# Optimization experiments

Hardware: AMD Instinct MI355X
Metric: run time of the kernel (lower is better)

Reference implementation:

```python
import jax, jax.numpy as jnp
import numpy as np

B, S, F, E, R, O = 4, 2048, 2048, 16, 16, 2048
TEMPERATURE = 1.0


def setup_inputs() -> dict:
    key = jax.random.key(0)
    k1, k2, k3, k4 = jax.random.split(key, 4)
    x = jax.random.normal(k1, (B, S, F), dtype=jnp.float32)
    prototypes = jax.random.normal(k2, (E, F), dtype=jnp.float32)
    # prototypes are top right-singular vectors -> unit norm rows
    prototypes = prototypes / jnp.linalg.norm(prototypes, axis=1, keepdims=True)
    A_stack = jax.random.normal(k3, (E, R, F), dtype=jnp.float32) * 0.02
    B_stack = jax.random.normal(k4, (E, O, R), dtype=jnp.float32) * 0.02
    scaling = jnp.float32(2.0)
    return {"x": x, "prototypes": prototypes, "A_stack": A_stack,
            "B_stack": B_stack, "scaling": scaling, "top_k": 4}


def reference(x, prototypes, A_stack, B_stack, scaling, top_k):
    lead = x.shape[:-1]
    f_in = x.shape[-1]
    tok = x.reshape(-1, f_in)                       # (t, F)
    t = tok.shape[0]

    # Arrow routing: abs cosine-like similarity to per-expert prototypes
    sim = jnp.abs(tok @ prototypes.T)               # (t, E)
    top_v, idx = jax.lax.top_k(sim, top_k)          # (t, k)
    full_score = jnp.full(sim.shape, -jnp.inf, dtype=sim.dtype)
    full_score = full_score.at[jnp.arange(t)[:, None], idx].set(top_v)
    coeff = jax.nn.softmax(full_score / TEMPERATURE, axis=1)  # (t, E), zeros off top-k

    # Per-expert LoRA: z = tok @ A_e^T  (dense over all experts, as in source)
    z = jnp.einsum('tf,erf->ter', tok, A_stack)     # (t, E, r)
    # Combine coeff into the low-rank space before the B projection to avoid
    # materializing the (t, E, out) tensor; math identical to
    # einsum('te, teo -> to', coeff, einsum('ter,eor->teo', z, B_stack)).
    delta = jnp.einsum('te,ter,eor->to', coeff, z, B_stack)  # (t, O)

    delta = scaling * delta                          # dropout = identity (eval)
    return delta.reshape(lead + (delta.shape[-1],))
```

## Files before the change

kernel.cpp:

```cpp
#include <hip/hip_runtime.h>
#include <hip/hip_bf16.h>
#include <stdint.h>

#define T_TOKENS 8192
#define F_DIM    2048
#define E_EXP    16
#define R_RANK   16
#define O_DIM    2048
#define KDIM     (E_EXP * R_RANK)

typedef short v8s __attribute__((ext_vector_type(8)));
typedef float v4f __attribute__((ext_vector_type(4)));

#define AS1 __attribute__((address_space(1)))
#define AS3 __attribute__((address_space(3)))

__device__ __forceinline__ uint16_t f2bf(float f) {
  uint32_t u = __builtin_bit_cast(uint32_t, f);
  u += 0x7fffu + ((u >> 16) & 1u);
  return (uint16_t)(u >> 16);
}

__device__ __forceinline__ void g2lds16(const uint16_t* g, uint16_t* l) {
  __builtin_amdgcn_global_load_lds((AS1 void*)g, (AS3 void*)l, 16, 0, 0);
}

__global__ __launch_bounds__(256) void prep_weights(
    const float* __restrict__ A, const float* __restrict__ Bst,
    uint16_t* __restrict__ Ab, uint16_t* __restrict__ Bb) {
  int idx = blockIdx.x * 256 + threadIdx.x;
  if (idx < KDIM * F_DIM) {
    Ab[idx] = f2bf(A[idx]);
  }
  if (idx < O_DIM * KDIM) {
    int k = idx & (KDIM - 1);
    int o = idx >> 8;
    int e = k >> 4, r = k & 15;
    Bb[idx] = f2bf(Bst[((size_t)e * O_DIM + o) * R_RANK + r]);
  }
}

__global__ __launch_bounds__(256) void route_stream(
    const float* __restrict__ x, const float* __restrict__ P,
    uint16_t* __restrict__ xb, float4* __restrict__ partials4) {
  __shared__ float ps[16 * 260];
  const int tid = threadIdx.x;
  const int c   = blockIdx.x;
  const int by  = blockIdx.y;
  const int f0  = c * 256;

  {
    const int e = tid >> 4;
    #pragma unroll
    for (int j = 0; j < 4; ++j) {
      const int col = (tid & 15) * 4 + j * 64;
      *(float4*)&ps[e * 260 + col] =
          *(const float4*)&P[(size_t)e * F_DIM + f0 + col];
    }
  }
  __syncthreads();

  const int sub = tid & 15;
  const int tg  = tid >> 4;
  const int t0  = by * 64 + tg * 4;
  const float* xr = x + (size_t)t0 * F_DIM + f0;
  uint16_t*    xw = xb + (size_t)t0 * F_DIM + f0;

  float a0[16], a1[16], a2[16], a3[16];
  #pragma unroll
  for (int e = 0; e < 16; ++e) { a0[e] = 0.f; a1[e] = 0.f; a2[e] = 0.f; a3[e] = 0.f; }

  #pragma unroll
  for (int j = 0; j < 4; ++j) {
    const int off = sub * 4 + j * 64;
    float4 v0 = *(const float4*)&xr[off];
    float4 v1 = *(const float4*)&xr[F_DIM + off];
    float4 v2 = *(const float4*)&xr[2 * F_DIM + off];
    float4 v3 = *(const float4*)&xr[3 * F_DIM + off];
    uint2 p0, p1, p2, p3;
    p0.x = (uint32_t)f2bf(v0.x) | ((uint32_t)f2bf(v0.y) << 16);
    p0.y = (uint32_t)f2bf(v0.z) | ((uint32_t)f2bf(v0.w) << 16);
    p1.x = (uint32_t)f2bf(v1.x) | ((uint32_t)f2bf(v1.y) << 16);
    p1.y = (uint32_t)f2bf(v1.z) | ((uint32_t)f2bf(v1.w) << 16);
    p2.x = (uint32_t)f2bf(v2.x) | ((uint32_t)f2bf(v2.y) << 16);
    p2.y = (uint32_t)f2bf(v2.z) | ((uint32_t)f2bf(v2.w) << 16);
    p3.x = (uint32_t)f2bf(v3.x) | ((uint32_t)f2bf(v3.y) << 16);
    p3.y = (uint32_t)f2bf(v3.z) | ((uint32_t)f2bf(v3.w) << 16);
    *(uint2*)&xw[off]             = p0;
    *(uint2*)&xw[F_DIM + off]     = p1;
    *(uint2*)&xw[2 * F_DIM + off] = p2;
    *(uint2*)&xw[3 * F_DIM + off] = p3;
    #pragma unroll
    for (int e = 0; e < 16; ++e) {
      float4 pv = *(float4*)&ps[e * 260 + off];
      a0[e] += v0.x * pv.x; a0[e] += v0.y * pv.y; a0[e] += v0.z * pv.z; a0[e] += v0.w * pv.w;
      a1[e] += v1.x * pv.x; a1[e] += v1.y * pv.y; a1[e] += v1.z * pv.z; a1[e] += v1.w * pv.w;
      a2[e] += v2.x * pv.x; a2[e] += v2.y * pv.y; a2[e] += v2.z * pv.z; a2[e] += v2.w * pv.w;
      a3[e] += v3.x * pv.x; a3[e] += v3.y * pv.y; a3[e] += v3.z * pv.z; a3[e] += v3.w * pv.w;
    }
  }

  #pragma unroll
  for (int e = 0; e < 16; ++e) {
    #pragma unroll
    for (int m = 1; m < 16; m <<= 1) {
      a0[e] += __shfl_xor(a0[e], m, 64);
      a1[e] += __shfl_xor(a1[e], m, 64);
      a2[e] += __shfl_xor(a2[e], m, 64);
      a3[e] += __shfl_xor(a3[e], m, 64);
    }
  }

  const size_t cb = (size_t)c * 4;
  if (sub == 0) {
    #pragma unroll
    for (int e4 = 0; e4 < 4; ++e4)
      partials4[(cb + e4) * T_TOKENS + t0] =
          make_float4(a0[e4 * 4], a0[e4 * 4 + 1], a0[e4 * 4 + 2], a0[e4 * 4 + 3]);
  } else if (sub == 1) {
    #pragma unroll
    for (int e4 = 0; e4 < 4; ++e4)
      partials4[(cb + e4) * T_TOKENS + t0 + 1] =
          make_float4(a1[e4 * 4], a1[e4 * 4 + 1], a1[e4 * 4 + 2], a1[e4 * 4 + 3]);
  } else if (sub == 2) {
    #pragma unroll
    for (int e4 = 0; e4 < 4; ++e4)
      partials4[(cb + e4) * T_TOKENS + t0 + 2] =
          make_float4(a2[e4 * 4], a2[e4 * 4 + 1], a2[e4 * 4 + 2], a2[e4 * 4 + 3]);
  } else if (sub == 3) {
    #pragma unroll
    for (int e4 = 0; e4 < 4; ++e4)
      partials4[(cb + e4) * T_TOKENS + t0 + 3] =
          make_float4(a3[e4 * 4], a3[e4 * 4 + 1], a3[e4 * 4 + 2], a3[e4 * 4 + 3]);
  }
}

__global__ __launch_bounds__(256) void route_topk(
    const float4* __restrict__ partials4, const float* __restrict__ scaling,
    const int* __restrict__ topk, float* __restrict__ coeffS) {
  const int t = blockIdx.x * 256 + threadIdx.x;
  double s[16];
  #pragma unroll
  for (int e = 0; e < 16; ++e) s[e] = 0.0;
  for (int c = 0; c < 8; ++c) {
    #pragma unroll
    for (int e4 = 0; e4 < 4; ++e4) {
      float4 p = partials4[((size_t)c * 4 + e4) * T_TOKENS + t];
      s[e4 * 4]     += (double)p.x;
      s[e4 * 4 + 1] += (double)p.y;
      s[e4 * 4 + 2] += (double)p.z;
      s[e4 * 4 + 3] += (double)p.w;
    }
  }
  double v[16];
  #pragma unroll
  for (int e = 0; e < 16; ++e) v[e] = fabs(s[e]);

  int k = topk[0];
  if (k > 16) k = 16;
  if (k < 1)  k = 1;
  unsigned mask = 0;
  double mx = 0.0;
  float ssum = 0.f;
  for (int i = 0; i < k; ++i) {
    double bv = -1.0; int bj = 0;
    #pragma unroll
    for (int j = 0; j < 16; ++j) {
      bool ok = !((mask >> j) & 1u) && (v[j] > bv);
      bv = ok ? v[j] : bv;
      bj = ok ? j  : bj;
    }
    mask |= 1u << bj;
    if (i == 0) mx = bv;
    ssum += expf((float)(bv - mx));
  }
  const float sc = scaling[0];
  float co[16];
  #pragma unroll
  for (int j = 0; j < 16; ++j)
    co[j] = ((mask >> j) & 1u) ? expf((float)(v[j] - mx)) / ssum * sc : 0.f;
  float* cw = coeffS + (size_t)t * 16;
  #pragma unroll
  for (int j4 = 0; j4 < 4; ++j4)
    *(float4*)&cw[j4 * 4] = make_float4(co[j4 * 4], co[j4 * 4 + 1],
                                        co[j4 * 4 + 2], co[j4 * 4 + 3]);
}

__global__ __launch_bounds__(256) void gemm_xa(
    const uint16_t* __restrict__ xb, const uint16_t* __restrict__ Ab,
    const float* __restrict__ coeffS, uint16_t* __restrict__ wb) {
  __shared__ uint16_t S[16384];
  uint16_t* Xh[2] = { S,         S + 4096  };
  uint16_t* Ah[2] = { S + 8192,  S + 12288 };
  const int tid  = threadIdx.x;
  const int n0   = blockIdx.x * 64;
  const int m0   = blockIdx.y * 64;
  const int lane = tid & 63;
  const int wid  = tid >> 6;
  const int wm   = (wid >> 1) * 32;
  const int wn   = (wid & 1) * 32;
  const int quad = lane >> 4;
  const int cl   = lane & 15;

  const int G0 = wid * 64 + lane;
  const int G1 = G0 + 256;
  const int r0 = G0 >> 3, g0 = (G0 & 7) ^ (r0 & 7);
  const int r1 = G1 >> 3, g1 = (G1 & 7) ^ (r1 & 7);
  const uint16_t* xs0 = xb + (size_t)(m0 + r0) * F_DIM + g0 * 8;
  const uint16_t* xs1 = xb + (size_t)(m0 + r1) * F_DIM + g1 * 8;
  const uint16_t* as0 = Ab + (size_t)(n0 + r0) * F_DIM + g0 * 8;
  const uint16_t* as1 = Ab + (size_t)(n0 + r1) * F_DIM + g1 * 8;
  const int d0 = wid * 512;
  const int d1 = wid * 512 + 2048;

  const int ma0 = wm + cl, ma1 = wm + 16 + cl;
  const int nb0 = wn + cl, nb1 = wn + 16 + cl;

  v4f acc[2][2];
  #pragma unroll
  for (int i = 0; i < 2; i++)
    #pragma unroll
    for (int j = 0; j < 2; j++) acc[i][j] = (v4f){0.f, 0.f, 0.f, 0.f};

  for (int k0 = 0; k0 < F_DIM; k0 += 128) {
    __syncthreads();
    g2lds16(xs0 + k0,      Xh[0] + d0);
    g2lds16(xs1 + k0,      Xh[0] + d1);
    g2lds16(as0 + k0,      Ah[0] + d0);
    g2lds16(as1 + k0,      Ah[0] + d1);
    g2lds16(xs0 + k0 + 64, Xh[1] + d0);
    g2lds16(xs1 + k0 + 64, Xh[1] + d1);
    g2lds16(as0 + k0 + 64, Ah[1] + d0);
    g2lds16(as1 + k0 + 64, Ah[1] + d1);
    __syncthreads();
    #pragma unroll
    for (int h = 0; h < 2; ++h) {
      #pragma unroll
      for (int ks = 0; ks < 2; ++ks) {
        const int gk = ks * 4 + quad;
        v8s fa0 = *(v8s*)&Xh[h][(ma0 * 8 + (gk ^ (ma0 & 7))) * 8];
        v8s fa1 = *(v8s*)&Xh[h][(ma1 * 8 + (gk ^ (ma1 & 7))) * 8];
        v8s fb0 = *(v8s*)&Ah[h][(nb0 * 8 + (gk ^ (nb0 & 7))) * 8];
        v8s fb1 = *(v8s*)&Ah[h][(nb1 * 8 + (gk ^ (nb1 & 7))) * 8];
        acc[0][0] = __builtin_amdgcn_mfma_f32_16x16x32_bf16(fa0, fb0, acc[0][0], 0, 0, 0);
        acc[0][1] = __builtin_amdgcn_mfma_f32_16x16x32_bf16(fa0, fb1, acc[0][1], 0, 0, 0);
        acc[1][0] = __builtin_amdgcn_mfma_f32_16x16x32_bf16(fa1, fb0, acc[1][0], 0, 0, 0);
        acc[1][1] = __builtin_amdgcn_mfma_f32_16x16x32_bf16(fa1, fb1, acc[1][1], 0, 0, 0);
      }
    }
  }

  __syncthreads();
  uint16_t* tile = S;
  #pragma unroll
  for (int mi = 0; mi < 2; mi++)
    #pragma unroll
    for (int ni = 0; ni < 2; ni++) {
      const int nl = wn + ni * 16 + cl;
      const int eidx = (n0 + nl) >> 4;
      #pragma unroll
      for (int reg = 0; reg < 4; reg++) {
        const int tl = wm + mi * 16 + quad * 4 + reg;
        float wv = acc[mi][ni][reg] * coeffS[(size_t)(m0 + tl) * 16 + eidx];
        tile[tl * 72 + nl] = f2bf(wv);
      }
    }
  __syncthreads();
  #pragma unroll
  for (int p = 0; p < 2; ++p) {
    const int row  = p * 32 + (tid >> 3);
    const int colg = (tid & 7) * 8;
    uint4 val = *(uint4*)&tile[row * 72 + colg];
    *(uint4*)&wb[(size_t)(m0 + row) * KDIM + n0 + colg] = val;
  }
}

__global__ __launch_bounds__(256) void gemm_wb(
    const uint16_t* __restrict__ wb, const uint16_t* __restrict__ Bb,
    float* __restrict__ out) {
  __shared__ uint16_t S[16384];
  uint16_t* Wh[2] = { S,         S + 4096  };
  uint16_t* Bh[2] = { S + 8192,  S + 12288 };
  const int tid  = threadIdx.x;
  const int n0   = blockIdx.x * 64;
  const int m0   = blockIdx.y * 64;
  const int lane = tid & 63;
  const int wid  = tid >> 6;
  const int wm   = (wid >> 1) * 32;
  const int wn   = (wid & 1) * 32;
  const int quad = lane >> 4;
  const int cl   = lane & 15;

  const int G0 = wid * 64 + lane;
  const int G1 = G0 + 256;
  const int r0 = G0 >> 3, g0 = (G0 & 7) ^ (r0 & 7);
  const int r1 = G1 >> 3, g1 = (G1 & 7) ^ (r1 & 7);
  const uint16_t* ws0 = wb + (size_t)(m0 + r0) * KDIM + g0 * 8;
  const uint16_t* ws1 = wb + (size_t)(m0 + r1) * KDIM + g1 * 8;
  const uint16_t* bs0 = Bb + (size_t)(n0 + r0) * KDIM + g0 * 8;
  const uint16_t* bs1 = Bb + (size_t)(n0 + r1) * KDIM + g1 * 8;
  const int d0 = wid * 512;
  const int d1 = wid * 512 + 2048;

  const int ma0 = wm + cl, ma1 = wm + 16 + cl;
  const int nb0 = wn + cl, nb1 = wn + 16 + cl;

  v4f acc[2][2];
  #pragma unroll
  for (int i = 0; i < 2; i++)
    #pragma unroll
    for (int j = 0; j < 2; j++) acc[i][j] = (v4f){0.f, 0.f, 0.f, 0.f};

  #pragma unroll
  for (int k0 = 0; k0 < KDIM; k0 += 128) {
    __syncthreads();
    g2lds16(ws0 + k0,      Wh[0] + d0);
    g2lds16(ws1 + k0,      Wh[0] + d1);
    g2lds16(bs0 + k0,      Bh[0] + d0);
    g2lds16(bs1 + k0,      Bh[0] + d1);
    g2lds16(ws0 + k0 + 64, Wh[1] + d0);
    g2lds16(ws1 + k0 + 64, Wh[1] + d1);
    g2lds16(bs0 + k0 + 64, Bh[1] + d0);
    g2lds16(bs1 + k0 + 64, Bh[1] + d1);
    __syncthreads();
    #pragma unroll
    for (int h = 0; h < 2; ++h) {
      #pragma unroll
      for (int ks = 0; ks < 2; ++ks) {
        const int gk = ks * 4 + quad;
        v8s fa0 = *(v8s*)&Wh[h][(ma0 * 8 + (gk ^ (ma0 & 7))) * 8];
        v8s fa1 = *(v8s*)&Wh[h][(ma1 * 8 + (gk ^ (ma1 & 7))) * 8];
        v8s fb0 = *(v8s*)&Bh[h][(nb0 * 8 + (gk ^ (nb0 & 7))) * 8];
        v8s fb1 = *(v8s*)&Bh[h][(nb1 * 8 + (gk ^ (nb1 & 7))) * 8];
        acc[0][0] = __builtin_amdgcn_mfma_f32_16x16x32_bf16(fa0, fb0, acc[0][0], 0, 0, 0);
        acc[0][1] = __builtin_amdgcn_mfma_f32_16x16x32_bf16(fa0, fb1, acc[0][1], 0, 0, 0);
        acc[1][0] = __builtin_amdgcn_mfma_f32_16x16x32_bf16(fa1, fb0, acc[1][0], 0, 0, 0);
        acc[1][1] = __builtin_amdgcn_mfma_f32_16x16x32_bf16(fa1, fb1, acc[1][1], 0, 0, 0);
      }
    }
  }

  __syncthreads();
  float* ft = (float*)S;
  #pragma unroll
  for (int mi = 0; mi < 2; mi++)
    #pragma unroll
    for (int ni = 0; ni < 2; ni++) {
      const int nl = wn + ni * 16 + cl;
      #pragma unroll
      for (int reg = 0; reg < 4; reg++) {
        const int tl = wm + mi * 16 + quad * 4 + reg;
        ft[tl * 68 + nl] = acc[mi][ni][reg];
      }
    }
  __syncthreads();
  #pragma unroll
  for (int p = 0; p < 4; ++p) {
    const int row = p * 16 + (tid >> 4);
    const int col = (tid & 15) * 4;
    float4 val = *(float4*)&ft[row * 68 + col];
    *(float4*)&out[(size_t)(m0 + row) * O_DIM + n0 + col] = val;
  }
}

extern "C" void kernel_launch(void* const* d_in, const int* in_sizes, int n_in,
                              void* d_out, int out_size, void* d_ws, size_t ws_size,
                              hipStream_t stream) {
  (void)in_sizes; (void)n_in; (void)out_size; (void)ws_size;
  const float* x       = (const float*)d_in[0];
  const float* P       = (const float*)d_in[1];
  const float* A       = (const float*)d_in[2];
  const float* Bst     = (const float*)d_in[3];
  const float* scaling = (const float*)d_in[4];
  const int*   topk    = (const int*)d_in[5];
  float* out = (float*)d_out;

  char* ws = (char*)d_ws;
  uint16_t* xb     = (uint16_t*)(ws);
  uint16_t* Ab     = (uint16_t*)(ws + 33554432);
  uint16_t* Bb     = (uint16_t*)(ws + 34603008);
  float4*   parts  = (float4*)  (ws + 35651584);
  uint16_t* wbuf   = (uint16_t*)(ws + 35651584);
  float*    coeffS = (float*)   (ws + 39845888);

  hipLaunchKernelGGL(prep_weights, dim3(2048), dim3(256), 0, stream, A, Bst, Ab, Bb);
  hipLaunchKernelGGL(route_stream, dim3(8, 128), dim3(256), 0, stream, x, P, xb, parts);
  hipLaunchKernelGGL(route_topk, dim3(T_TOKENS / 256), dim3(256), 0, stream,
                     parts, scaling, topk, coeffS);
  hipLaunchKernelGGL(gemm_xa, dim3(KDIM / 64, T_TOKENS / 64), dim3(256), 0, stream,
                     xb, Ab, coeffS, wbuf);
  hipLaunchKernelGGL(gemm_wb, dim3(O_DIM / 64, T_TOKENS / 64), dim3(256), 0, stream,
                     wbuf, Bb, out);
}
```

Baseline: 189.3 us.

## Fuse top-k routing into XA GEMM and widen WB GEMM tiles with swizzled grid

Removes the separate route_topk kernel: each gemm_xa block recomputes the top-k softmax coefficients for its 64 tokens into shared memory, dropping one launch and the coeffS round trip through global memory. gemm_wb moves from 64x64 to 64x256 output tiles with a 1-D swizzled block index, so each W tile is loaded once per 256 columns and L2 locality improves, at the cost of more accumulator registers. It also uses a single-buffer K=64 step and a two-pass epilogue through shared memory. Routing work is now repeated across the 4 N-blocks of gemm_xa for the same tokens, and the partials buffer moved so it no longer aliases wbuf.

```diff
diff --git a/kernel.cpp b/kernel.cpp
--- a/kernel.cpp
+++ b/kernel.cpp
@@ -135,72 +135,68 @@
   }
 }
 
-__global__ __launch_bounds__(256) void route_topk(
-    const float4* __restrict__ partials4, const float* __restrict__ scaling,
-    const int* __restrict__ topk, float* __restrict__ coeffS) {
-  const int t = blockIdx.x * 256 + threadIdx.x;
-  double s[16];
-  #pragma unroll
-  for (int e = 0; e < 16; ++e) s[e] = 0.0;
-  for (int c = 0; c < 8; ++c) {
-    #pragma unroll
-    for (int e4 = 0; e4 < 4; ++e4) {
-      float4 p = partials4[((size_t)c * 4 + e4) * T_TOKENS + t];
-      s[e4 * 4]     += (double)p.x;
-      s[e4 * 4 + 1] += (double)p.y;
-      s[e4 * 4 + 2] += (double)p.z;
-      s[e4 * 4 + 3] += (double)p.w;
-    }
-  }
-  double v[16];
-  #pragma unroll
-  for (int e = 0; e < 16; ++e) v[e] = fabs(s[e]);
-
-  int k = topk[0];
-  if (k > 16) k = 16;
-  if (k < 1)  k = 1;
-  unsigned mask = 0;
-  double mx = 0.0;
-  float ssum = 0.f;
-  for (int i = 0; i < k; ++i) {
-    double bv = -1.0; int bj = 0;
-    #pragma unroll
-    for (int j = 0; j < 16; ++j) {
-      bool ok = !((mask >> j) & 1u) && (v[j] > bv);
-      bv = ok ? v[j] : bv;
-      bj = ok ? j  : bj;
-    }
-    mask |= 1u << bj;
-    if (i == 0) mx = bv;
-    ssum += expf((float)(bv - mx));
-  }
-  const float sc = scaling[0];
-  float co[16];
-  #pragma unroll
-  for (int j = 0; j < 16; ++j)
-    co[j] = ((mask >> j) & 1u) ? expf((float)(v[j] - mx)) / ssum * sc : 0.f;
-  float* cw = coeffS + (size_t)t * 16;
-  #pragma unroll
-  for (int j4 = 0; j4 < 4; ++j4)
-    *(float4*)&cw[j4 * 4] = make_float4(co[j4 * 4], co[j4 * 4 + 1],
-                                        co[j4 * 4 + 2], co[j4 * 4 + 3]);
-}
-
 __global__ __launch_bounds__(256) void gemm_xa(
     const uint16_t* __restrict__ xb, const uint16_t* __restrict__ Ab,
-    const float* __restrict__ coeffS, uint16_t* __restrict__ wb) {
+    const float4* __restrict__ partials4, const float* __restrict__ scaling,
+    const int* __restrict__ topk, uint16_t* __restrict__ wb) {
   __shared__ uint16_t S[16384];
+  __shared__ float coeffL[64 * 17];
   uint16_t* Xh[2] = { S,         S + 4096  };
   uint16_t* Ah[2] = { S + 8192,  S + 12288 };
   const int tid  = threadIdx.x;
-  const int n0   = blockIdx.x * 64;
-  const int m0   = blockIdx.y * 64;
+  const int b    = blockIdx.x;
+  const int m_idx = (b & 7) + ((b >> 5) << 3);
+  const int n_idx = (b >> 3) & 3;
+  const int m0 = m_idx * 64, n0 = n_idx * 64;
   const int lane = tid & 63;
   const int wid  = tid >> 6;
   const int wm   = (wid >> 1) * 32;
   const int wn   = (wid & 1) * 32;
   const int quad = lane >> 4;
   const int cl   = lane & 15;
+
+  if (tid < 64) {
+    const int t = m0 + tid;
+    double s[16];
+    #pragma unroll
+    for (int e = 0; e < 16; ++e) s[e] = 0.0;
+    for (int c = 0; c < 8; ++c) {
+      #pragma unroll
+      for (int e4 = 0; e4 < 4; ++e4) {
+        float4 p = partials4[((size_t)c * 4 + e4) * T_TOKENS + t];
+        s[e4 * 4]     += (double)p.x;
+        s[e4 * 4 + 1] += (double)p.y;
+        s[e4 * 4 + 2] += (double)p.z;
+        s[e4 * 4 + 3] += (double)p.w;
+      }
+    }
+    double v[16];
+    #pragma unroll
+    for (int e = 0; e < 16; ++e) v[e] = fabs(s[e]);
+    int k = topk[0];
+    if (k > 16) k = 16;
+    if (k < 1)  k = 1;
+    unsigned mask = 0;
+    double mx = 0.0;
+    float ssum = 0.f;
+    for (int i = 0; i < k; ++i) {
+      double bv = -1.0; int bj = 0;
+      #pragma unroll
+      for (int j = 0; j < 16; ++j) {
+        bool ok = !((mask >> j) & 1u) && (v[j] > bv);
+        bv = ok ? v[j] : bv;
+        bj = ok ? j  : bj;
+      }
+      mask |= 1u << bj;
+      if (i == 0) mx = bv;
+      ssum += expf((float)(bv - mx));
+    }
+    const float sc = scaling[0];
+    #pragma unroll
+    for (int j = 0; j < 16; ++j)
+      coeffL[tid * 17 + j] = ((mask >> j) & 1u)
+          ? expf((float)(v[j] - mx)) / ssum * sc : 0.f;
+  }
 
   const int G0 = wid * 64 + lane;
   const int G1 = G0 + 256;
@@ -261,7 +257,7 @@
       #pragma unroll
       for (int reg = 0; reg < 4; reg++) {
         const int tl = wm + mi * 16 + quad * 4 + reg;
-        float wv = acc[mi][ni][reg] * coeffS[(size_t)(m0 + tl) * 16 + eidx];
+        float wv = acc[mi][ni][reg] * coeffL[tl * 17 + eidx];
         tile[tl * 72 + nl] = f2bf(wv);
       }
     }
@@ -276,90 +272,101 @@
 }
 
 __global__ __launch_bounds__(256) void gemm_wb(
-    const uint16_t* __restrict__ wb, const uint16_t* __restrict__ Bb,
+    const uint16_t* __restrict__ wbuf, const uint16_t* __restrict__ Bb,
     float* __restrict__ out) {
-  __shared__ uint16_t S[16384];
-  uint16_t* Wh[2] = { S,         S + 4096  };
-  uint16_t* Bh[2] = { S + 8192,  S + 12288 };
+  __shared__ uint16_t S[20480];
+  uint16_t* Ws = S;
+  uint16_t* Bs = S + 4096;
   const int tid  = threadIdx.x;
-  const int n0   = blockIdx.x * 64;
-  const int m0   = blockIdx.y * 64;
+  const int b    = blockIdx.x;
+  const int m_idx = (b & 7) + ((b >> 6) << 3);
+  const int n_idx = (b >> 3) & 7;
+  const int m0 = m_idx * 64;
+  const int n0 = n_idx * 256;
   const int lane = tid & 63;
   const int wid  = tid >> 6;
   const int wm   = (wid >> 1) * 32;
-  const int wn   = (wid & 1) * 32;
+  const int wn   = (wid & 1) * 128;
   const int quad = lane >> 4;
   const int cl   = lane & 15;
 
-  const int G0 = wid * 64 + lane;
-  const int G1 = G0 + 256;
-  const int r0 = G0 >> 3, g0 = (G0 & 7) ^ (r0 & 7);
-  const int r1 = G1 >> 3, g1 = (G1 & 7) ^ (r1 & 7);
-  const uint16_t* ws0 = wb + (size_t)(m0 + r0) * KDIM + g0 * 8;
-  const uint16_t* ws1 = wb + (size_t)(m0 + r1) * KDIM + g1 * 8;
-  const uint16_t* bs0 = Bb + (size_t)(n0 + r0) * KDIM + g0 * 8;
-  const uint16_t* bs1 = Bb + (size_t)(n0 + r1) * KDIM + g1 * 8;
-  const int d0 = wid * 512;
-  const int d1 = wid * 512 + 2048;
+  const int GW0 = wid * 64 + lane;
+  const int GW1 = GW0 + 256;
+  const int wr0 = GW0 >> 3, wg0 = (GW0 & 7) ^ (wr0 & 7);
+  const int wr1 = GW1 >> 3, wg1 = (GW1 & 7) ^ (wr1 & 7);
+  const uint16_t* wsrc0 = wbuf + (size_t)(m0 + wr0) * KDIM + wg0 * 8;
+  const uint16_t* wsrc1 = wbuf + (size_t)(m0 + wr1) * KDIM + wg1 * 8;
+
+  const uint16_t* bsrc[8];
+  #pragma unroll
+  for (int p = 0; p < 8; ++p) {
+    const int G = p * 256 + wid * 64 + lane;
+    const int r = G >> 3, g = (G & 7) ^ (r & 7);
+    bsrc[p] = Bb + (size_t)(n0 + r) * KDIM + g * 8;
+  }
+
+  v4f acc[2][8];
+  #pragma unroll
+  for (int i = 0; i < 2; i++)
+    #pragma unroll
+    for (int j = 0; j < 8; j++) acc[i][j] = (v4f){0.f, 0.f, 0.f, 0.f};
 
   const int ma0 = wm + cl, ma1 = wm + 16 + cl;
-  const int nb0 = wn + cl, nb1 = wn + 16 + cl;
-
-  v4f acc[2][2];
-  #pragma unroll
-  for (int i = 0; i < 2; i++)
-    #pragma unroll
-    for (int j = 0; j < 2; j++) acc[i][j] = (v4f){0.f, 0.f, 0.f, 0.f};
-
-  #pragma unroll
-  for (int k0 = 0; k0 < KDIM; k0 += 128) {
-    __syncthreads();
-    g2lds16(ws0 + k0,      Wh[0] + d0);
-    g2lds16(ws1 + k0,      Wh[0] + d1);
-    g2lds16(bs0 + k0,      Bh[0] + d0);
-    g2lds16(bs1 + k0,      Bh[0] + d1);
-    g2lds16(ws0 + k0 + 64, Wh[1] + d0);
-    g2lds16(ws1 + k0 + 64, Wh[1] + d1);
-    g2lds16(bs0 + k0 + 64, Bh[1] + d0);
-    g2lds16(bs1 + k0 + 64, Bh[1] + d1);
-    __syncthreads();
-    #pragma unroll
-    for (int h = 0; h < 2; ++h) {
-      #pragma unroll
-      for (int ks = 0; ks < 2; ++ks) {
-        const int gk = ks * 4 + quad;
-        v8s fa0 = *(v8s*)&Wh[h][(ma0 * 8 + (gk ^ (ma0 & 7))) * 8];
-        v8s fa1 = *(v8s*)&Wh[h][(ma1 * 8 + (gk ^ (ma1 & 7))) * 8];
-        v8s fb0 = *(v8s*)&Bh[h][(nb0 * 8 + (gk ^ (nb0 & 7))) * 8];
-        v8s fb1 = *(v8s*)&Bh[h][(nb1 * 8 + (gk ^ (nb1 & 7))) * 8];
-        acc[0][0] = __builtin_amdgcn_mfma_f32_16x16x32_bf16(fa0, fb0, acc[0][0], 0, 0, 0);
-        acc[0][1] = __builtin_amdgcn_mfma_f32_16x16x32_bf16(fa0, fb1, acc[0][1], 0, 0, 0);
-        acc[1][0] = __builtin_amdgcn_mfma_f32_16x16x32_bf16(fa1, fb0, acc[1][0], 0, 0, 0);
-        acc[1][1] = __builtin_amdgcn_mfma_f32_16x16x32_bf16(fa1, fb1, acc[1][1], 0, 0, 0);
-      }
-    }
-  }
-
-  __syncthreads();
+
+  #pragma unroll
+  for (int k0 = 0; k0 < KDIM; k0 += 64) {
+    __syncthreads();
+    g2lds16(wsrc0 + k0, Ws + wid * 512);
+    g2lds16(wsrc1 + k0, Ws + wid * 512 + 2048);
+    #pragma unroll
+    for (int p = 0; p < 8; ++p)
+      g2lds16(bsrc[p] + k0, Bs + (p * 256 + wid * 64) * 8);
+    __syncthreads();
+    #pragma unroll
+    for (int ks = 0; ks < 2; ++ks) {
+      const int gk = ks * 4 + quad;
+      v8s fa0 = *(v8s*)&Ws[(ma0 * 8 + (gk ^ (ma0 & 7))) * 8];
+      v8s fa1 = *(v8s*)&Ws[(ma1 * 8 + (gk ^ (ma1 & 7))) * 8];
+      v8s fb[8];
+      #pragma unroll
+      for (int j = 0; j < 8; ++j) {
+        const int nb = wn + j * 16 + cl;
+        fb[j] = *(v8s*)&Bs[(nb * 8 + (gk ^ (nb & 7))) * 8];
+      }
+      #pragma unroll
+      for (int j = 0; j < 8; ++j) {
+        acc[0][j] = __builtin_amdgcn_mfma_f32_16x16x32_bf16(fa0, fb[j], acc[0][j], 0, 0, 0);
+        acc[1][j] = __builtin_amdgcn_mfma_f32_16x16x32_bf16(fa1, fb[j], acc[1][j], 0, 0, 0);
+      }
+    }
+  }
+
   float* ft = (float*)S;
   #pragma unroll
-  for (int mi = 0; mi < 2; mi++)
-    #pragma unroll
-    for (int ni = 0; ni < 2; ni++) {
-      const int nl = wn + ni * 16 + cl;
-      #pragma unroll
-      for (int reg = 0; reg < 4; reg++) {
-        const int tl = wm + mi * 16 + quad * 4 + reg;
-        ft[tl * 68 + nl] = acc[mi][ni][reg];
-      }
-    }
-  __syncthreads();
-  #pragma unroll
-  for (int p = 0; p < 4; ++p) {
-    const int row = p * 16 + (tid >> 4);
-    const int col = (tid & 15) * 4;
-    float4 val = *(float4*)&ft[row * 68 + col];
-    *(float4*)&out[(size_t)(m0 + row) * O_DIM + n0 + col] = val;
+  for (int h = 0; h < 2; ++h) {
+    __syncthreads();
+    if ((wid >> 1) == h) {
+      #pragma unroll
+      for (int mi = 0; mi < 2; mi++)
+        #pragma unroll
+        for (int j = 0; j < 8; j++) {
+          const int col = wn + j * 16 + cl;
+          #pragma unroll
+          for (int reg = 0; reg < 4; reg++) {
+            const int rl = mi * 16 + quad * 4 + reg;
+            ft[rl * 260 + col] = acc[mi][j][reg];
+          }
+        }
+    }
+    __syncthreads();
+    #pragma unroll
+    for (int p = 0; p < 8; ++p) {
+      const int f4  = p * 256 + tid;
+      const int row = f4 >> 6;
+      const int c4  = f4 & 63;
+      float4 v = *(float4*)&ft[row * 260 + c4 * 4];
+      *(float4*)&out[(size_t)(m0 + h * 32 + row) * O_DIM + n0 + c4 * 4] = v;
+    }
   }
 }
 
@@ -379,16 +386,12 @@
   uint16_t* xb     = (uint16_t*)(ws);
   uint16_t* Ab     = (uint16_t*)(ws + 33554432);
   uint16_t* Bb     = (uint16_t*)(ws + 34603008);
-  float4*   parts  = (float4*)  (ws + 35651584);
   uint16_t* wbuf   = (uint16_t*)(ws + 35651584);
-  float*    coeffS = (float*)   (ws + 39845888);
+  float4*   parts  = (float4*)  (ws + 39845888);
 
   hipLaunchKernelGGL(prep_weights, dim3(2048), dim3(256), 0, stream, A, Bst, Ab, Bb);
   hipLaunchKernelGGL(route_stream, dim3(8, 128), dim3(256), 0, stream, x, P, xb, parts);
-  hipLaunchKernelGGL(route_topk, dim3(T_TOKENS / 256), dim3(256), 0, stream,
-                     parts, scaling, topk, coeffS);
-  hipLaunchKernelGGL(gemm_xa, dim3(KDIM / 64, T_TOKENS / 64), dim3(256), 0, stream,
-                     xb, Ab, coeffS, wbuf);
-  hipLaunchKernelGGL(gemm_wb, dim3(O_DIM / 64, T_TOKENS / 64), dim3(256), 0, stream,
-                     wbuf, Bb, out);
-}
+  hipLaunchKernelGGL(gemm_xa, dim3(512), dim3(256), 0, stream,
+                     xb, Ab, parts, scaling, topk, wbuf);
+  hipLaunchKernelGGL(gemm_wb, dim3(1024), dim3(256), 0, stream, wbuf, Bb, out);
+}
```

Result: faster. 167.7 us (-11.5%).
